# Kernel optimization log

Measured on AMD Instinct MI355X. Metric: run time of the kernel, lower is better.

The kernel has to match this reference:

```python
import jax, jax.numpy as jnp
import numpy as np

N_AGENTS = 8
N_HEADS = 4
HYP = 128   # hypernet_embed
EMB = 32    # mixing_embed_dim


def _hypernet(entities, entity_mask, fc1_w, fc1_b, attn_w, out_w, out_b, fc2_w, fc2_b):
    # entities: [B, ne, ed]; entity_mask: [B, ne] (1 = masked/inactive)
    B, ne, _ = entities.shape
    hd = HYP // N_HEADS
    x1 = jax.nn.relu(entities @ fc1_w + fc1_b)                      # [B, ne, HYP]
    am = entity_mask[:, :N_AGENTS].astype(x1.dtype)                 # [B, na]
    em = entity_mask.astype(x1.dtype)                               # [B, ne]
    # attn_mask[b,i,j] = 1 - (1-am[i])*(1-em[j]): mask if agent i OR entity j inactive
    pre_mask = 1.0 - (1.0 - am)[:, :, None] * (1.0 - em)[:, None, :]  # [B, na, ne]
    # EntityAttentionLayer: agents are the queries, all entities are keys/values
    qkv = x1 @ attn_w                                               # [B, ne, 3*HYP] (no bias)
    q, k, v = jnp.split(qkv, 3, axis=-1)
    q = q[:, :N_AGENTS].reshape(B, N_AGENTS, N_HEADS, hd)
    k = k.reshape(B, ne, N_HEADS, hd)
    v = v.reshape(B, ne, N_HEADS, hd)
    scale = jnp.asarray(np.sqrt(hd), x1.dtype)
    logits = jnp.einsum('bqhd,bkhd->bhqk', q, k) / scale            # [B, H, na, ne]
    m = pre_mask[:, None, :, :]
    # masked softmax; fully-masked rows (torch: -inf -> NaN -> 0) become 0 via *(1-m)
    w = jax.nn.softmax(jnp.where(m > 0, -1e30, logits), axis=-1) * (1.0 - m)
    attn = jnp.einsum('bhqk,bkhd->bqhd', w, v).reshape(B, N_AGENTS, HYP)
    attn = attn @ out_w + out_b                                     # [B, na, HYP]
    keep = (1.0 - am)[:, :, None]                                   # zero masked agents (post_mask)
    attn = attn * keep
    x3 = (attn @ fc2_w + fc2_b) * keep                              # [B, na, EMB]
    return x3


def reference(agent_qs, entities, entity_mask, fc1_w, fc1_b, attn_w, out_w, out_b, fc2_w, fc2_b):
    bs, T, ne, ed = entities.shape
    B = bs * T
    ents = entities.reshape(B, ne, ed)
    emask = entity_mask.reshape(B, ne)
    qs = agent_qs.reshape(B, N_AGENTS)
    # 4 hypernets: 0=hyper_w_1 (matrix), 1=hyper_w_final (vector), 2=hyper_b_1 (vector), 3=V (scalar)
    outs = [_hypernet(ents, emask, fc1_w[i], fc1_b[i], attn_w[i], out_w[i],
                      out_b[i], fc2_w[i], fc2_b[i]) for i in range(4)]
    w1 = jax.nn.softmax(outs[0], axis=-1)                           # [B, na, EMB]
    b1 = outs[2].mean(axis=1)                                       # [B, EMB]
    hidden = jax.nn.elu(jnp.einsum('ba,bae->be', qs, w1) + b1)      # [B, EMB]
    w_final = jax.nn.softmax(outs[1].mean(axis=1), axis=-1)         # [B, EMB]
    v = outs[3].mean(axis=(1, 2))                                   # [B]
    y = jnp.sum(hidden * w_final, axis=-1) + v                      # [B]
    return y.reshape(bs, T, 1)


def setup_inputs() -> dict:
    key = jax.random.key(0)
    ks = jax.random.split(key, 10)
    bs, T, ne, ed = 128, 64, 16, 64
    s = 0.05
    return {
        'agent_qs': jax.random.normal(ks[0], (bs, T, N_AGENTS), jnp.float32),
        'entities': jax.random.normal(ks[1], (bs, T, ne, ed), jnp.float32),
        'entity_mask': jax.random.randint(ks[2], (bs, T, ne), 0, 2, jnp.int32),
        'fc1_w': jax.random.normal(ks[3], (4, ed, HYP), jnp.float32) * s,
        'fc1_b': jax.random.normal(ks[4], (4, HYP), jnp.float32) * s,
        'attn_w': jax.random.normal(ks[5], (4, HYP, 3 * HYP), jnp.float32) * s,
        'out_w': jax.random.normal(ks[6], (4, HYP, HYP), jnp.float32) * s,
        'out_b': jax.random.normal(ks[7], (4, HYP), jnp.float32) * s,
        'fc2_w': jax.random.normal(ks[8], (4, HYP, EMB), jnp.float32) * s,
        'fc2_b': jax.random.normal(ks[9], (4, EMB), jnp.float32) * s,
    }
```

## Files before the change

kernel.cpp:

```cpp
#include <hip/hip_runtime.h>
#include <math.h>

#define NAG 8
#define NE  16
#define ED  64
#define HYPD 128
#define QKVW 384
#define SB 4

#define X1S 132
#define KVS 260
#define QS  132

#define OFF_X1    0
#define OFF_SLOG  0
#define OFF_ATTN  8448
#define OFF_KV    16896
#define OFF_ATTN2 16896
#define OFF_Q     50176
#define OFF_OUT0  58624
#define OFF_MEANS 60672
#define OFF_EM    62208
#define LDS_BYTES 62464

typedef __attribute__((ext_vector_type(8))) short bf16x8;
typedef __attribute__((ext_vector_type(4))) short bf16x4;
typedef __attribute__((ext_vector_type(4))) float f32x4;

__device__ __forceinline__ short f2bf(float f) {
    union { float f; unsigned u; } c; c.f = f;
    unsigned r = (c.u + 0x7FFFu + ((c.u >> 16) & 1u)) >> 16;
    return (short)r;
}
__device__ __forceinline__ float bf2f(short s) {
    union { unsigned u; float f; } c; c.u = ((unsigned)(unsigned short)s) << 16; return c.f;
}
__device__ __forceinline__ bf16x8 ld_frag(const short* p) {
    bf16x4 lo = *(const bf16x4*)p;
    bf16x4 hi = *(const bf16x4*)(p + 16);
    return __builtin_shufflevector(lo, hi, 0, 1, 2, 3, 4, 5, 6, 7);
}

__global__ void pack_weights(const float* __restrict__ fc1_w,
                             const float* __restrict__ attn_w,
                             const float* __restrict__ out_w,
                             const float* __restrict__ fc2_w,
                             short* __restrict__ ws) {
    int gid = blockIdx.x * 256 + threadIdx.x;
    if (gid >= 608 * 64) return;
    int slot = gid >> 6, l = gid & 63;
    const float* src; int N, nt, kt;
    if (slot < 64) {
        int h = slot >> 4, f = slot & 15;
        nt = f >> 1; kt = f & 1; N = HYPD; src = fc1_w + h * ED * HYPD;
    } else if (slot < 448) {
        int s2 = slot - 64; int h = s2 / 96, f = s2 % 96;
        nt = f >> 2; kt = f & 3; N = QKVW; src = attn_w + h * HYPD * QKVW;
    } else if (slot < 576) {
        int s2 = slot - 448; int h = s2 >> 5, f = s2 & 31;
        nt = f >> 2; kt = f & 3; N = HYPD; src = out_w + h * HYPD * HYPD;
    } else {
        int s2 = slot - 576; int h = s2 >> 3, f = s2 & 7;
        nt = f >> 2; kt = f & 3; N = 32; src = fc2_w + h * HYPD * 32;
    }
    int rg = l >> 4, lc = l & 15;
    bf16x8 fr;
    #pragma unroll
    for (int j = 0; j < 8; ++j) {
        int k = kt * 32 + 4 * rg + (j & 3) + 16 * (j >> 2);
        fr[j] = f2bf(src[k * N + nt * 16 + lc]);
    }
    ((bf16x8*)ws)[slot * 64 + l] = fr;
}

__global__ __launch_bounds__(256, 2) void flexq_mfma(
    const float* __restrict__ agent_qs,
    const float* __restrict__ entities,
    const int*   __restrict__ entity_mask,
    const float* __restrict__ fc1_b,
    const float* __restrict__ out_b,
    const float* __restrict__ fc2_b,
    const short* __restrict__ wfrag,
    float* __restrict__ out, int B)
{
    __shared__ __align__(16) char smem[LDS_BYTES];
    short* x1    = (short*)(smem + OFF_X1);
    float* slog  = (float*)(smem + OFF_SLOG);
    short* attn  = (short*)(smem + OFF_ATTN);
    short* kv    = (short*)(smem + OFF_KV);
    short* attn2 = (short*)(smem + OFF_ATTN2);
    short* q     = (short*)(smem + OFF_Q);
    short* out0  = (short*)(smem + OFF_OUT0);
    float* means = (float*)(smem + OFF_MEANS);
    float* em    = (float*)(smem + OFF_EM);

    const int tid = threadIdx.x;
    const int l = tid & 63, w = tid >> 6;
    const int rg = l >> 4, lc = l & 15;
    const int b4 = blockIdx.x * SB;
    const bf16x8* WF = (const bf16x8*)wfrag;

    if (tid < 64)
        em[tid] = (entity_mask[(size_t)b4 * NE + tid] != 0) ? 1.0f : 0.0f;

    bf16x8 aent[2][4];
    #pragma unroll
    for (int kt = 0; kt < 2; ++kt)
        #pragma unroll
        for (int mt = 0; mt < 4; ++mt) {
            const float* ap = entities + ((size_t)(b4 + mt) * NE + lc) * ED + kt * 32 + rg * 4;
            float4 lo = *(const float4*)ap;
            float4 hi = *(const float4*)(ap + 16);
            bf16x8 af;
            af[0]=f2bf(lo.x); af[1]=f2bf(lo.y); af[2]=f2bf(lo.z); af[3]=f2bf(lo.w);
            af[4]=f2bf(hi.x); af[5]=f2bf(hi.y); af[6]=f2bf(hi.z); af[7]=f2bf(hi.w);
            aent[kt][mt] = af;
        }
    __syncthreads();

    for (int i = 0; i < 4; ++i) {
        {
            f32x4 acc[4][2];
            #pragma unroll
            for (int mt = 0; mt < 4; ++mt) {
                acc[mt][0] = (f32x4){0.f,0.f,0.f,0.f};
                acc[mt][1] = (f32x4){0.f,0.f,0.f,0.f};
            }
            #pragma unroll
            for (int kt = 0; kt < 2; ++kt) {
                bf16x8 b0 = WF[(i*16 + (2*w+0)*2 + kt)*64 + l];
                bf16x8 b1 = WF[(i*16 + (2*w+1)*2 + kt)*64 + l];
                #pragma unroll
                for (int mt = 0; mt < 4; ++mt) {
                    acc[mt][0] = __builtin_amdgcn_mfma_f32_16x16x32_bf16(aent[kt][mt], b0, acc[mt][0], 0,0,0);
                    acc[mt][1] = __builtin_amdgcn_mfma_f32_16x16x32_bf16(aent[kt][mt], b1, acc[mt][1], 0,0,0);
                }
            }
            float bias0 = fc1_b[i*HYPD + 32*w + lc];
            float bias1 = fc1_b[i*HYPD + 32*w + 16 + lc];
            #pragma unroll
            for (int mt = 0; mt < 4; ++mt)
                #pragma unroll
                for (int r = 0; r < 4; ++r) {
                    int row = 16*mt + 4*rg + r;
                    x1[row*X1S + 32*w + lc]      = f2bf(fmaxf(acc[mt][0][r] + bias0, 0.f));
                    x1[row*X1S + 32*w + 16 + lc] = f2bf(fmaxf(acc[mt][1][r] + bias1, 0.f));
                }
        }
        __syncthreads();

        #pragma unroll
        for (int hf = 0; hf < 2; ++hf) {
            f32x4 acc[4][3];
            #pragma unroll
            for (int mt = 0; mt < 4; ++mt)
                #pragma unroll
                for (int n = 0; n < 3; ++n) acc[mt][n] = (f32x4){0.f,0.f,0.f,0.f};
            #pragma unroll
            for (int kt = 0; kt < 4; ++kt) {
                bf16x8 b0 = WF[(64 + i*96 + (6*w + 3*hf + 0)*4 + kt)*64 + l];
                bf16x8 b1 = WF[(64 + i*96 + (6*w + 3*hf + 1)*4 + kt)*64 + l];
                bf16x8 b2 = WF[(64 + i*96 + (6*w + 3*hf + 2)*4 + kt)*64 + l];
                #pragma unroll
                for (int mt = 0; mt < 4; ++mt) {
                    bf16x8 a = ld_frag(x1 + (16*mt + lc)*X1S + kt*32 + rg*4);
                    acc[mt][0] = __builtin_amdgcn_mfma_f32_16x16x32_bf16(a, b0, acc[mt][0], 0,0,0);
                    acc[mt][1] = __builtin_amdgcn_mfma_f32_16x16x32_bf16(a, b1, acc[mt][1], 0,0,0);
                    acc[mt][2] = __builtin_amdgcn_mfma_f32_16x16x32_bf16(a, b2, acc[mt][2], 0,0,0);
                }
            }
            #pragma unroll
            for (int n = 0; n < 3; ++n) {
                int nt = 6*w + 3*hf + n;
                int col = nt * 16 + lc;
                #pragma unroll
                for (int mt = 0; mt < 4; ++mt)
                    #pragma unroll
                    for (int r = 0; r < 4; ++r) {
                        short v = f2bf(acc[mt][n][r]);
                        if (nt < 8) {
                            if (rg < 2) q[(mt*NAG + 4*rg + r)*QS + col] = v;
                        } else {
                            kv[(16*mt + 4*rg + r)*KVS + (col - HYPD)] = v;
                        }
                    }
            }
        }
        __syncthreads();

        {
            #pragma unroll
            for (int pp = 0; pp < 4; ++pp) {
                int p = 4*w + pp, s = p >> 2, h = p & 3;
                bf16x8 a  = ld_frag(q  + (s*NAG + (lc & 7))*QS + h*32 + rg*4);
                bf16x8 bb = ld_frag(kv + (s*NE  + lc)*KVS       + h*32 + rg*4);
                f32x4 acc = (f32x4){0.f,0.f,0.f,0.f};
                acc = __builtin_amdgcn_mfma_f32_16x16x32_bf16(a, bb, acc, 0,0,0);
                if (rg < 2) {
                    #pragma unroll
                    for (int r = 0; r < 4; ++r)
                        slog[((s*4 + h)*NAG + 4*rg + r)*16 + lc] = acc[r] * 0.17677669529663687f;
                }
            }
        }
        __syncthreads();

        if (tid < 128) {
            int s = tid >> 5, h = (tid >> 3) & 3, qi = tid & 7;
            float am = em[s*NE + qi];
            float* rowp = slog + ((s*4 + h)*NAG + qi)*16;
            float mx = -3.0e38f; bool any = false;
            #pragma unroll
            for (int k = 0; k < NE; ++k)
                if (em[s*NE + k] == 0.f) { any = true; mx = fmaxf(mx, rowp[k]); }
            if (am != 0.f || !any) {
                #pragma unroll
                for (int k = 0; k < NE; ++k) rowp[k] = 0.f;
            } else {
                float eb[NE]; float sum = 0.f;
                #pragma unroll
                for (int k = 0; k < NE; ++k) {
                    float e = (em[s*NE + k] == 0.f) ? __expf(rowp[k] - mx) : 0.f;
                    eb[k] = e; sum += e;
                }
                float inv = 1.f / sum;
                #pragma unroll
                for (int k = 0; k < NE; ++k) rowp[k] = eb[k] * inv;
            }
        }
        __syncthreads();

        {
            #pragma unroll
            for (int pp = 0; pp < 4; ++pp) {
                int p = 4*w + pp, s = p >> 2, h = p & 3;
                f32x4 pw = *(const f32x4*)(slog + ((s*4 + h)*NAG + (lc & 7))*16 + 4*rg);
                bf16x8 a;
                a[0]=f2bf(pw[0]); a[1]=f2bf(pw[1]); a[2]=f2bf(pw[2]); a[3]=f2bf(pw[3]);
                a[4]=0; a[5]=0; a[6]=0; a[7]=0;
                #pragma unroll
                for (int d0 = 0; d0 < 2; ++d0) {
                    bf16x8 bb;
                    #pragma unroll
                    for (int j = 0; j < 4; ++j)
                        bb[j] = kv[(s*NE + 4*rg + j)*KVS + 128 + h*32 + d0*16 + lc];
                    bb[4]=0; bb[5]=0; bb[6]=0; bb[7]=0;
                    f32x4 acc = (f32x4){0.f,0.f,0.f,0.f};
                    acc = __builtin_amdgcn_mfma_f32_16x16x32_bf16(a, bb, acc, 0,0,0);
                    if (rg < 2) {
                        #pragma unroll
                        for (int r = 0; r < 4; ++r)
                            attn[(s*NAG + 4*rg + r)*X1S + h*32 + d0*16 + lc] = f2bf(acc[r]);
                    }
                }
            }
        }
        __syncthreads();

        {
            f32x4 acc[2][2];
            #pragma unroll
            for (int mt = 0; mt < 2; ++mt) {
                acc[mt][0] = (f32x4){0.f,0.f,0.f,0.f};
                acc[mt][1] = (f32x4){0.f,0.f,0.f,0.f};
            }
            #pragma unroll
            for (int kt = 0; kt < 4; ++kt) {
                bf16x8 b0 = WF[(448 + i*32 + (2*w+0)*4 + kt)*64 + l];
                bf16x8 b1 = WF[(448 + i*32 + (2*w+1)*4 + kt)*64 + l];
                #pragma unroll
                for (int mt = 0; mt < 2; ++mt) {
                    bf16x8 a = ld_frag(attn + (16*mt + lc)*X1S + kt*32 + rg*4);
                    acc[mt][0] = __builtin_amdgcn_mfma_f32_16x16x32_bf16(a, b0, acc[mt][0], 0,0,0);
                    acc[mt][1] = __builtin_amdgcn_mfma_f32_16x16x32_bf16(a, b1, acc[mt][1], 0,0,0);
                }
            }
            float bias0 = out_b[i*HYPD + 32*w + lc];
            float bias1 = out_b[i*HYPD + 32*w + 16 + lc];
            #pragma unroll
            for (int mt = 0; mt < 2; ++mt)
                #pragma unroll
                for (int r = 0; r < 4; ++r) {
                    int row = 16*mt + 4*rg + r;
                    float keep = 1.f - em[(row >> 3)*NE + (row & 7)];
                    attn2[row*X1S + 32*w + lc]      = f2bf((acc[mt][0][r] + bias0) * keep);
                    attn2[row*X1S + 32*w + 16 + lc] = f2bf((acc[mt][1][r] + bias1) * keep);
                }
        }
        __syncthreads();

        {
            int mt = w >> 1, nt = w & 1;
            f32x4 acc = (f32x4){0.f,0.f,0.f,0.f};
            #pragma unroll
            for (int kt = 0; kt < 4; ++kt) {
                bf16x8 a = ld_frag(attn2 + (16*mt + lc)*X1S + kt*32 + rg*4);
                bf16x8 bfr = WF[(576 + i*8 + nt*4 + kt)*64 + l];
                acc = __builtin_amdgcn_mfma_f32_16x16x32_bf16(a, bfr, acc, 0,0,0);
            }
            float bias = fc2_b[i*32 + nt*16 + lc];
            float vals[4];
            #pragma unroll
            for (int r = 0; r < 4; ++r) {
                int row = 16*mt + 4*rg + r;
                float keep = 1.f - em[(row >> 3)*NE + (row & 7)];
                vals[r] = (acc[r] + bias) * keep;
            }
            if (i == 0) {
                #pragma unroll
                for (int r = 0; r < 4; ++r)
                    out0[(16*mt + 4*rg + r)*32 + nt*16 + lc] = f2bf(vals[r]);
            } else {
                float ps = vals[0] + vals[1] + vals[2] + vals[3];
                ps += __shfl_xor(ps, 16);
                if ((rg & 1) == 0) {
                    int s = 2*mt + (rg >> 1);
                    means[(i-1)*128 + s*32 + nt*16 + lc] = ps;
                }
            }
        }
        __syncthreads();
    }

    if (l < 32) {
        int s = w, c = l;
        float s1 = means[0*128 + s*32 + c] * 0.125f;
        float b1 = means[1*128 + s*32 + c] * 0.125f;
        float vsum = means[2*128 + s*32 + c];

        float hid = 0.f;
        #pragma unroll
        for (int a = 0; a < NAG; ++a) {
            float x = bf2f(out0[(s*NAG + a)*32 + c]);
            float mx = x;
            #pragma unroll
            for (int m = 16; m >= 1; m >>= 1) mx = fmaxf(mx, __shfl_xor(mx, m, 32));
            float e = __expf(x - mx);
            float sum = e;
            #pragma unroll
            for (int m = 16; m >= 1; m >>= 1) sum += __shfl_xor(sum, m, 32);
            float qsv = agent_qs[(size_t)(b4 + s)*NAG + a];
            hid += qsv * (e / sum);
        }
        hid += b1;
        hid = (hid > 0.f) ? hid : expm1f(hid);

        float mx = s1;
        #pragma unroll
        for (int m = 16; m >= 1; m >>= 1) mx = fmaxf(mx, __shfl_xor(mx, m, 32));
        float e = __expf(s1 - mx);
        float ss = e;
        #pragma unroll
        for (int m = 16; m >= 1; m >>= 1) ss += __shfl_xor(ss, m, 32);
        float wf = e / ss;

        float red = hid * wf + vsum * (1.f / 256.f);
        #pragma unroll
        for (int m = 16; m >= 1; m >>= 1) red += __shfl_xor(red, m, 32);
        if (c == 0) out[b4 + s] = red;
    }
}

#define QKVP 388
#define NTHR 384
__device__ __forceinline__ float4 f4load(const float* p) { return *reinterpret_cast<const float4*>(p); }
__device__ __forceinline__ void f4store(float* p, const float4& v) { *reinterpret_cast<float4*>(p) = v; }
__device__ __forceinline__ void f4fma(float4& a, float s, const float4& w) {
    a.x += s * w.x; a.y += s * w.y; a.z += s * w.z; a.w += s * w.w;
}

__global__ __launch_bounds__(NTHR) void flexq_fp32(
    const float* __restrict__ agent_qs, const float* __restrict__ entities,
    const int* __restrict__ entity_mask, const float* __restrict__ fc1_w,
    const float* __restrict__ fc1_b, const float* __restrict__ attn_w,
    const float* __restrict__ out_w, const float* __restrict__ out_b,
    const float* __restrict__ fc2_w, const float* __restrict__ fc2_b,
    float* __restrict__ out)
{
    const int b = blockIdx.x, tid = threadIdx.x;
    __shared__ float s_ent[NE][ED];
    __shared__ float s_x1t[HYPD][NE];
    __shared__ float s_qkv[NE][QKVP];
    __shared__ float s_w[4][NAG][NE];
    __shared__ float s_attn[NAG][HYPD];
    __shared__ float s_attnout[NAG][HYPD];
    __shared__ float s_outs[4][NAG][32];
    __shared__ float s_mask[NE];
    __shared__ float s_qs[NAG];

    const float* ent = entities + (size_t)b * NE * ED;
    for (int o = tid; o < NE * ED; o += NTHR) s_ent[o >> 6][o & 63] = ent[o];
    if (tid < NE) s_mask[tid] = (entity_mask[(size_t)b * NE + tid] != 0) ? 1.0f : 0.0f;
    if (tid < NAG) s_qs[tid] = agent_qs[(size_t)b * NAG + tid];
    __syncthreads();

    for (int i = 0; i < 4; ++i) {
        {
            const float* W1 = fc1_w + i * ED * HYPD;
            const float* B1 = fc1_b + i * HYPD;
            for (int o4 = tid; o4 < 512; o4 += NTHR) {
                int e = o4 >> 5, j = (o4 & 31) * 4;
                float4 acc = f4load(B1 + j);
                for (int d = 0; d < ED; ++d) { float x = s_ent[e][d]; f4fma(acc, x, f4load(W1 + d * HYPD + j)); }
                s_x1t[j+0][e] = fmaxf(acc.x, 0.f); s_x1t[j+1][e] = fmaxf(acc.y, 0.f);
                s_x1t[j+2][e] = fmaxf(acc.z, 0.f); s_x1t[j+3][e] = fmaxf(acc.w, 0.f);
            }
        }
        __syncthreads();
        {
            const float* W2 = attn_w + i * HYPD * QKVW;
            int j = (tid % 96) * 4, e0 = (tid / 96) * 4;
            float4 a0 = {0,0,0,0}, a1 = {0,0,0,0}, a2 = {0,0,0,0}, a3 = {0,0,0,0};
            for (int d = 0; d < HYPD; ++d) {
                float4 wv = f4load(W2 + d * QKVW + j);
                float4 x = f4load(&s_x1t[d][e0]);
                f4fma(a0, x.x, wv); f4fma(a1, x.y, wv); f4fma(a2, x.z, wv); f4fma(a3, x.w, wv);
            }
            f4store(&s_qkv[e0+0][j], a0); f4store(&s_qkv[e0+1][j], a1);
            f4store(&s_qkv[e0+2][j], a2); f4store(&s_qkv[e0+3][j], a3);
        }
        __syncthreads();
        {
            const float inv_scale = 0.17677669529663687f;
            for (int o = tid; o < 512; o += NTHR) {
                int h = o >> 7, qi = (o >> 4) & 7, k = o & 15;
                const float* qp = &s_qkv[qi][h * 32];
                const float* kp = &s_qkv[k][HYPD + h * 32];
                float s = 0.f;
                #pragma unroll
                for (int d4 = 0; d4 < 8; ++d4) {
                    float4 qv = f4load(qp + 4 * d4), kk = f4load(kp + 4 * d4);
                    s += qv.x*kk.x + qv.y*kk.y + qv.z*kk.z + qv.w*kk.w;
                }
                s_w[h][qi][k] = s * inv_scale;
            }
        }
        __syncthreads();
        if (tid < 32) {
            int h = tid >> 3, qi = tid & 7;
            float am = s_mask[qi];
            float mx = -3.0e38f; bool any = false;
            #pragma unroll
            for (int k = 0; k < NE; ++k)
                if (s_mask[k] == 0.f) { any = true; mx = fmaxf(mx, s_w[h][qi][k]); }
            if (am != 0.f || !any) {
                #pragma unroll
                for (int k = 0; k < NE; ++k) s_w[h][qi][k] = 0.f;
            } else {
                float eb[NE]; float sum = 0.f;
                #pragma unroll
                for (int k = 0; k < NE; ++k) {
                    float e = (s_mask[k] == 0.f) ? __expf(s_w[h][qi][k] - mx) : 0.f;
                    eb[k] = e; sum += e;
                }
                float inv = 1.f / sum;
                #pragma unroll
                for (int k = 0; k < NE; ++k) s_w[h][qi][k] = eb[k] * inv;
            }
        }
        __syncthreads();
        if (tid < 256) {
            int qi = tid >> 5, j = (tid & 31) * 4, h = j >> 5, d0 = j & 31;
            float4 acc = {0,0,0,0};
            #pragma unroll
            for (int k = 0; k < NE; ++k) f4fma(acc, s_w[h][qi][k], f4load(&s_qkv[k][2*HYPD + h*32 + d0]));
            f4store(&s_attn[qi][j], acc);
        }
        __syncthreads();
        if (tid < 256) {
            const float* W3 = out_w + i * HYPD * HYPD;
            const float* B3 = out_b + i * HYPD;
            int qi = tid >> 5, j = (tid & 31) * 4;
            float4 acc = f4load(B3 + j);
            for (int d = 0; d < HYPD; ++d) f4fma(acc, s_attn[qi][d], f4load(W3 + d * HYPD + j));
            float keep = 1.f - s_mask[qi];
            acc.x *= keep; acc.y *= keep; acc.z *= keep; acc.w *= keep;
            f4store(&s_attnout[qi][j], acc);
        }
        __syncthreads();
        if (tid < 64) {
            const float* W4 = fc2_w + i * HYPD * 32;
            const float* B4 = fc2_b + i * 32;
            int qi = tid >> 3, c = (tid & 7) * 4;
            float4 acc = f4load(B4 + c);
            for (int d = 0; d < HYPD; ++d) f4fma(acc, s_attnout[qi][d], f4load(W4 + d * 32 + c));
            float keep = 1.f - s_mask[qi];
            acc.x *= keep; acc.y *= keep; acc.z *= keep; acc.w *= keep;
            f4store(&s_outs[i][qi][c], acc);
        }
        __syncthreads();
    }

    if (tid < 32) {
        const int c = tid;
        float b1 = 0.f, s1 = 0.f, vs = 0.f;
        #pragma unroll
        for (int qi = 0; qi < NAG; ++qi) {
            b1 += s_outs[2][qi][c]; s1 += s_outs[1][qi][c]; vs += s_outs[3][qi][c];
        }
        b1 *= 0.125f; s1 *= 0.125f;
        float hid = 0.f;
        #pragma unroll
        for (int a = 0; a < NAG; ++a) {
            float x = s_outs[0][a][c];
            float mx = x;
            #pragma unroll
            for (int m = 16; m >= 1; m >>= 1) mx = fmaxf(mx, __shfl_xor(mx, m, 32));
            float e = __expf(x - mx);
            float sm = e;
            #pragma unroll
            for (int m = 16; m >= 1; m >>= 1) sm += __shfl_xor(sm, m, 32);
            hid += s_qs[a] * (e / sm);
        }
        hid += b1;
        hid = (hid > 0.f) ? hid : expm1f(hid);
        float mx = s1;
        #pragma unroll
        for (int m = 16; m >= 1; m >>= 1) mx = fmaxf(mx, __shfl_xor(mx, m, 32));
        float e = __expf(s1 - mx);
        float ssum = e;
        #pragma unroll
        for (int m = 16; m >= 1; m >>= 1) ssum += __shfl_xor(ssum, m, 32);
        float wf = e / ssum;
        float red = hid * wf + vs * (1.f / 256.f);
        #pragma unroll
        for (int m = 16; m >= 1; m >>= 1) red += __shfl_xor(red, m, 32);
        if (tid == 0) out[b] = red;
    }
}

extern "C" void kernel_launch(void* const* d_in, const int* in_sizes, int n_in,
                              void* d_out, int out_size, void* d_ws, size_t ws_size,
                              hipStream_t stream) {
    const float* agent_qs    = (const float*)d_in[0];
    const float* entities    = (const float*)d_in[1];
    const int*   entity_mask = (const int*)  d_in[2];
    const float* fc1_w       = (const float*)d_in[3];
    const float* fc1_b       = (const float*)d_in[4];
    const float* attn_w      = (const float*)d_in[5];
    const float* out_w       = (const float*)d_in[6];
    const float* out_b       = (const float*)d_in[7];
    const float* fc2_w       = (const float*)d_in[8];
    const float* fc2_b       = (const float*)d_in[9];
    float* out = (float*)d_out;

    const int B = in_sizes[0] / NAG;

    if (ws_size >= (size_t)(608 * 1024) && (B % SB) == 0) {
        pack_weights<<<152, 256, 0, stream>>>(fc1_w, attn_w, out_w, fc2_w, (short*)d_ws);
        flexq_mfma<<<B / SB, 256, 0, stream>>>(agent_qs, entities, entity_mask,
                                               fc1_b, out_b, fc2_b,
                                               (const short*)d_ws, out, B);
    } else {
        flexq_fp32<<<B, NTHR, 0, stream>>>(agent_qs, entities, entity_mask,
                                           fc1_w, fc1_b, attn_w, out_w, out_b,
                                           fc2_w, fc2_b, out);
    }
}
```

Measured before the change: 222.7 us.

## Keep V projection in registers and shrink LDS for three blocks per CU

The QKV projection is repartitioned so each wave computes V column tiles whose MFMA output layout matches the B-operand layout of the attention-times-V MFMA. The V accumulators then stay in registers and are converted directly, removing the V half of the LDS kv buffer and its strided scalar reads. LDS drops from about 62KB to 46KB and launch bounds are raised to 3 blocks per SM to increase occupancy. In exchange, V accumulators stay live across the softmax phase, adding register pressure that may cause spills under the tighter 3-block bound.

```diff
diff --git a/kernel.cpp b/kernel.cpp
--- a/kernel.cpp
+++ b/kernel.cpp
@@ -9,19 +9,19 @@
 #define SB 4
 
 #define X1S 132
-#define KVS 260
+#define KS  132
 #define QS  132
 
 #define OFF_X1    0
 #define OFF_SLOG  0
 #define OFF_ATTN  8448
-#define OFF_KV    16896
+#define OFF_K     16896
 #define OFF_ATTN2 16896
-#define OFF_Q     50176
-#define OFF_OUT0  58624
-#define OFF_MEANS 60672
-#define OFF_EM    62208
-#define LDS_BYTES 62464
+#define OFF_Q     33792
+#define OFF_OUT0  42240
+#define OFF_MEANS 44288
+#define OFF_EM    45824
+#define LDS_BYTES 46080
 
 typedef __attribute__((ext_vector_type(8))) short bf16x8;
 typedef __attribute__((ext_vector_type(4))) short bf16x4;
@@ -73,7 +73,7 @@
     ((bf16x8*)ws)[slot * 64 + l] = fr;
 }
 
-__global__ __launch_bounds__(256, 2) void flexq_mfma(
+__global__ __launch_bounds__(256, 3) void flexq_mfma(
     const float* __restrict__ agent_qs,
     const float* __restrict__ entities,
     const int*   __restrict__ entity_mask,
@@ -87,7 +87,7 @@
     short* x1    = (short*)(smem + OFF_X1);
     float* slog  = (float*)(smem + OFF_SLOG);
     short* attn  = (short*)(smem + OFF_ATTN);
-    short* kv    = (short*)(smem + OFF_KV);
+    short* k     = (short*)(smem + OFF_K);
     short* attn2 = (short*)(smem + OFF_ATTN2);
     short* q     = (short*)(smem + OFF_Q);
     short* out0  = (short*)(smem + OFF_OUT0);
@@ -149,8 +149,8 @@
         }
         __syncthreads();
 
-        #pragma unroll
-        for (int hf = 0; hf < 2; ++hf) {
+        f32x4 accv[4][2];
+        {
             f32x4 acc[4][3];
             #pragma unroll
             for (int mt = 0; mt < 4; ++mt)
@@ -158,9 +158,9 @@
                 for (int n = 0; n < 3; ++n) acc[mt][n] = (f32x4){0.f,0.f,0.f,0.f};
             #pragma unroll
             for (int kt = 0; kt < 4; ++kt) {
-                bf16x8 b0 = WF[(64 + i*96 + (6*w + 3*hf + 0)*4 + kt)*64 + l];
-                bf16x8 b1 = WF[(64 + i*96 + (6*w + 3*hf + 1)*4 + kt)*64 + l];
-                bf16x8 b2 = WF[(64 + i*96 + (6*w + 3*hf + 2)*4 + kt)*64 + l];
+                bf16x8 b0 = WF[(64 + i*96 + (w +  0)*4 + kt)*64 + l];
+                bf16x8 b1 = WF[(64 + i*96 + (w +  4)*4 + kt)*64 + l];
+                bf16x8 b2 = WF[(64 + i*96 + (w +  8)*4 + kt)*64 + l];
                 #pragma unroll
                 for (int mt = 0; mt < 4; ++mt) {
                     bf16x8 a = ld_frag(x1 + (16*mt + lc)*X1S + kt*32 + rg*4);
@@ -170,21 +170,42 @@
                 }
             }
             #pragma unroll
-            for (int n = 0; n < 3; ++n) {
-                int nt = 6*w + 3*hf + n;
-                int col = nt * 16 + lc;
-                #pragma unroll
-                for (int mt = 0; mt < 4; ++mt)
-                    #pragma unroll
-                    for (int r = 0; r < 4; ++r) {
-                        short v = f2bf(acc[mt][n][r]);
-                        if (nt < 8) {
-                            if (rg < 2) q[(mt*NAG + 4*rg + r)*QS + col] = v;
-                        } else {
-                            kv[(16*mt + 4*rg + r)*KVS + (col - HYPD)] = v;
-                        }
+            for (int mt = 0; mt < 4; ++mt)
+                #pragma unroll
+                for (int r = 0; r < 4; ++r) {
+                    if (rg < 2) {
+                        q[(mt*NAG + 4*rg + r)*QS + (w+0)*16 + lc] = f2bf(acc[mt][0][r]);
+                        q[(mt*NAG + 4*rg + r)*QS + (w+4)*16 + lc] = f2bf(acc[mt][1][r]);
                     }
-            }
+                    k[(16*mt + 4*rg + r)*KS + w*16 + lc] = f2bf(acc[mt][2][r]);
+                }
+        }
+        {
+            f32x4 acck[4];
+            #pragma unroll
+            for (int mt = 0; mt < 4; ++mt) {
+                acck[mt] = (f32x4){0.f,0.f,0.f,0.f};
+                accv[mt][0] = (f32x4){0.f,0.f,0.f,0.f};
+                accv[mt][1] = (f32x4){0.f,0.f,0.f,0.f};
+            }
+            #pragma unroll
+            for (int kt = 0; kt < 4; ++kt) {
+                bf16x8 b0 = WF[(64 + i*96 + (w + 12)*4 + kt)*64 + l];
+                bf16x8 b1 = WF[(64 + i*96 + (w + 16)*4 + kt)*64 + l];
+                bf16x8 b2 = WF[(64 + i*96 + (w + 20)*4 + kt)*64 + l];
+                #pragma unroll
+                for (int mt = 0; mt < 4; ++mt) {
+                    bf16x8 a = ld_frag(x1 + (16*mt + lc)*X1S + kt*32 + rg*4);
+                    acck[mt]    = __builtin_amdgcn_mfma_f32_16x16x32_bf16(a, b0, acck[mt], 0,0,0);
+                    accv[mt][0] = __builtin_amdgcn_mfma_f32_16x16x32_bf16(a, b1, accv[mt][0], 0,0,0);
+                    accv[mt][1] = __builtin_amdgcn_mfma_f32_16x16x32_bf16(a, b2, accv[mt][1], 0,0,0);
+                }
+            }
+            #pragma unroll
+            for (int mt = 0; mt < 4; ++mt)
+                #pragma unroll
+                for (int r = 0; r < 4; ++r)
+                    k[(16*mt + 4*rg + r)*KS + (w+4)*16 + lc] = f2bf(acck[mt][r]);
         }
         __syncthreads();
 
@@ -192,8 +213,8 @@
             #pragma unroll
             for (int pp = 0; pp < 4; ++pp) {
                 int p = 4*w + pp, s = p >> 2, h = p & 3;
-                bf16x8 a  = ld_frag(q  + (s*NAG + (lc & 7))*QS + h*32 + rg*4);
-                bf16x8 bb = ld_frag(kv + (s*NE  + lc)*KVS       + h*32 + rg*4);
+                bf16x8 a  = ld_frag(q + (s*NAG + (lc & 7))*QS + h*32 + rg*4);
+                bf16x8 bb = ld_frag(k + (s*NE  + lc)*KS       + h*32 + rg*4);
                 f32x4 acc = (f32x4){0.f,0.f,0.f,0.f};
                 acc = __builtin_amdgcn_mfma_f32_16x16x32_bf16(a, bb, acc, 0,0,0);
                 if (rg < 2) {
@@ -211,46 +232,46 @@
             float* rowp = slog + ((s*4 + h)*NAG + qi)*16;
             float mx = -3.0e38f; bool any = false;
             #pragma unroll
-            for (int k = 0; k < NE; ++k)
-                if (em[s*NE + k] == 0.f) { any = true; mx = fmaxf(mx, rowp[k]); }
+            for (int kk = 0; kk < NE; ++kk)
+                if (em[s*NE + kk] == 0.f) { any = true; mx = fmaxf(mx, rowp[kk]); }
             if (am != 0.f || !any) {
                 #pragma unroll
-                for (int k = 0; k < NE; ++k) rowp[k] = 0.f;
+                for (int kk = 0; kk < NE; ++kk) rowp[kk] = 0.f;
             } else {
                 float eb[NE]; float sum = 0.f;
                 #pragma unroll
-                for (int k = 0; k < NE; ++k) {
-                    float e = (em[s*NE + k] == 0.f) ? __expf(rowp[k] - mx) : 0.f;
-                    eb[k] = e; sum += e;
+                for (int kk = 0; kk < NE; ++kk) {
+                    float e = (em[s*NE + kk] == 0.f) ? __expf(rowp[kk] - mx) : 0.f;
+                    eb[kk] = e; sum += e;
                 }
                 float inv = 1.f / sum;
                 #pragma unroll
-                for (int k = 0; k < NE; ++k) rowp[k] = eb[k] * inv;
-            }
-        }
-        __syncthreads();
-
-        {
-            #pragma unroll
-            for (int pp = 0; pp < 4; ++pp) {
-                int p = 4*w + pp, s = p >> 2, h = p & 3;
-                f32x4 pw = *(const f32x4*)(slog + ((s*4 + h)*NAG + (lc & 7))*16 + 4*rg);
-                bf16x8 a;
-                a[0]=f2bf(pw[0]); a[1]=f2bf(pw[1]); a[2]=f2bf(pw[2]); a[3]=f2bf(pw[3]);
-                a[4]=0; a[5]=0; a[6]=0; a[7]=0;
-                #pragma unroll
-                for (int d0 = 0; d0 < 2; ++d0) {
+                for (int kk = 0; kk < NE; ++kk) rowp[kk] = eb[kk] * inv;
+            }
+        }
+        __syncthreads();
+
+        {
+            #pragma unroll
+            for (int vt = 0; vt < 2; ++vt) {
+                int c = w + 4*vt;
+                int h = c >> 1;
+                #pragma unroll
+                for (int mt = 0; mt < 4; ++mt) {
+                    f32x4 pw = *(const f32x4*)(slog + ((mt*4 + h)*NAG + (lc & 7))*16 + 4*rg);
+                    bf16x8 a;
+                    a[0]=f2bf(pw[0]); a[1]=f2bf(pw[1]); a[2]=f2bf(pw[2]); a[3]=f2bf(pw[3]);
+                    a[4]=0; a[5]=0; a[6]=0; a[7]=0;
                     bf16x8 bb;
-                    #pragma unroll
-                    for (int j = 0; j < 4; ++j)
-                        bb[j] = kv[(s*NE + 4*rg + j)*KVS + 128 + h*32 + d0*16 + lc];
+                    bb[0]=f2bf(accv[mt][vt][0]); bb[1]=f2bf(accv[mt][vt][1]);
+                    bb[2]=f2bf(accv[mt][vt][2]); bb[3]=f2bf(accv[mt][vt][3]);
                     bb[4]=0; bb[5]=0; bb[6]=0; bb[7]=0;
-                    f32x4 acc = (f32x4){0.f,0.f,0.f,0.f};
-                    acc = __builtin_amdgcn_mfma_f32_16x16x32_bf16(a, bb, acc, 0,0,0);
+                    f32x4 po = (f32x4){0.f,0.f,0.f,0.f};
+                    po = __builtin_amdgcn_mfma_f32_16x16x32_bf16(a, bb, po, 0,0,0);
                     if (rg < 2) {
                         #pragma unroll
                         for (int r = 0; r < 4; ++r)
-                            attn[(s*NAG + 4*rg + r)*X1S + h*32 + d0*16 + lc] = f2bf(acc[r]);
+                            attn[(mt*NAG + 4*rg + r)*X1S + c*16 + lc] = f2bf(po[r]);
                     }
                 }
             }
@@ -423,16 +444,16 @@
         {
             const float inv_scale = 0.17677669529663687f;
             for (int o = tid; o < 512; o += NTHR) {
-                int h = o >> 7, qi = (o >> 4) & 7, k = o & 15;
+                int h = o >> 7, qi = (o >> 4) & 7, kk = o & 15;
                 const float* qp = &s_qkv[qi][h * 32];
-                const float* kp = &s_qkv[k][HYPD + h * 32];
+                const float* kp = &s_qkv[kk][HYPD + h * 32];
                 float s = 0.f;
                 #pragma unroll
                 for (int d4 = 0; d4 < 8; ++d4) {
-                    float4 qv = f4load(qp + 4 * d4), kk = f4load(kp + 4 * d4);
-                    s += qv.x*kk.x + qv.y*kk.y + qv.z*kk.z + qv.w*kk.w;
-                }
-                s_w[h][qi][k] = s * inv_scale;
+                    float4 qv = f4load(qp + 4 * d4), kv2 = f4load(kp + 4 * d4);
+                    s += qv.x*kv2.x + qv.y*kv2.y + qv.z*kv2.z + qv.w*kv2.w;
+                }
+                s_w[h][qi][kk] = s * inv_scale;
             }
         }
         __syncthreads();
@@ -441,21 +462,21 @@
             float am = s_mask[qi];
             float mx = -3.0e38f; bool any = false;
             #pragma unroll
-            for (int k = 0; k < NE; ++k)
-                if (s_mask[k] == 0.f) { any = true; mx = fmaxf(mx, s_w[h][qi][k]); }
+            for (int kk = 0; kk < NE; ++kk)
+                if (s_mask[kk] == 0.f) { any = true; mx = fmaxf(mx, s_w[h][qi][kk]); }
             if (am != 0.f || !any) {
                 #pragma unroll
-                for (int k = 0; k < NE; ++k) s_w[h][qi][k] = 0.f;
+                for (int kk = 0; kk < NE; ++kk) s_w[h][qi][kk] = 0.f;
             } else {
                 float eb[NE]; float sum = 0.f;
                 #pragma unroll
-                for (int k = 0; k < NE; ++k) {
-                    float e = (s_mask[k] == 0.f) ? __expf(s_w[h][qi][k] - mx) : 0.f;
-                    eb[k] = e; sum += e;
+                for (int kk = 0; kk < NE; ++kk) {
+                    float e = (s_mask[kk] == 0.f) ? __expf(s_w[h][qi][kk] - mx) : 0.f;
+                    eb[kk] = e; sum += e;
                 }
                 float inv = 1.f / sum;
                 #pragma unroll
-                for (int k = 0; k < NE; ++k) s_w[h][qi][k] = eb[k] * inv;
+                for (int kk = 0; kk < NE; ++kk) s_w[h][qi][kk] = eb[kk] * inv;
             }
         }
         __syncthreads();
@@ -463,7 +484,7 @@
             int qi = tid >> 5, j = (tid & 31) * 4, h = j >> 5, d0 = j & 31;
             float4 acc = {0,0,0,0};
             #pragma unroll
-            for (int k = 0; k < NE; ++k) f4fma(acc, s_w[h][qi][k], f4load(&s_qkv[k][2*HYPD + h*32 + d0]));
+            for (int kk = 0; kk < NE; ++kk) f4fma(acc, s_w[h][qi][kk], f4load(&s_qkv[kk][2*HYPD + h*32 + d0]));
             f4store(&s_attn[qi][j], acc);
         }
         __syncthreads();
```

Measured after the change: 207.4 us. 1.07x faster.
